# Optimization experiments

Hardware: AMD Instinct MI355X
Metric: run time of the kernel (lower is better)

Reference implementation:

```python
import jax, jax.numpy as jnp
import numpy as np

BN_EPS = 1e-5


def setup_inputs() -> dict:
    key = jax.random.key(0)
    ks = jax.random.split(key, 4)
    B, C, N = 16, 512, 4096
    Cr = C // 4
    x = jax.random.normal(ks[0], (B, C, N), dtype=jnp.float32)
    W1 = jax.random.normal(ks[1], (Cr, C), dtype=jnp.float32) * (1.0 / np.sqrt(C))
    W2 = jax.random.normal(ks[2], (C, Cr), dtype=jnp.float32) * (1.0 / np.sqrt(Cr))
    gamma = jnp.ones((Cr,), dtype=jnp.float32)
    beta = jnp.zeros((Cr,), dtype=jnp.float32)
    running_mean = jnp.zeros((Cr,), dtype=jnp.float32)
    running_var = jnp.ones((Cr,), dtype=jnp.float32)
    return {"x": x, "W1": W1, "gamma": gamma, "beta": beta,
            "running_mean": running_mean, "running_var": running_var, "W2": W2}


def reference(x, W1, gamma, beta, running_mean, running_var, W2):
    # att[b,c] = sum_j (x x^T)[b,c,j] = sum_n x[b,c,n] * s[b,n], s = colsum over channels.
    # Algebraically identical to bmm(x, x^T).sum(-1), avoids the [B,C,C] intermediate.
    s = jnp.sum(x, axis=1)                       # [B, N]
    att = jnp.einsum('bcn,bn->bc', x, s)         # [B, C]
    # 1x1 Conv1d (no bias) on a length-1 sequence == dense matmul.
    h = jnp.einsum('oc,bc->bo', W1, att)         # [B, C/4]
    # BatchNorm1d (inference mode, running statistics)
    h = gamma * (h - running_mean) * jax.lax.rsqrt(running_var + BN_EPS) + beta
    h = jax.nn.relu(h)
    a = jax.nn.sigmoid(jnp.einsum('oc,bc->bo', W2, h))  # [B, C]
    return x * a[:, :, None]                     # [B, C, N]
```

## Files before the change

### kernel.cpp

```cpp
#include <hip/hip_runtime.h>
#include <math.h>

#define B_   16
#define C_   512
#define CR_  128
#define N_   4096
#define N4_  (N_ / 4)
#define TN   32
#define TN4  (TN / 4)
#define SUBT 2
#define NTB  (N_ / TN / SUBT)

static constexpr float BN_EPS_F = 1e-5f;

typedef float vfloat4 __attribute__((ext_vector_type(4)));

__global__ __launch_bounds__(256) void k1f_att(
        const float* __restrict__ x,
        float* __restrict__ att_part) {
    const int ntb = blockIdx.x;
    const int b   = blockIdx.y;
    const int t   = threadIdx.x;
    const int g   = t >> 3;
    const int i   = t & 7;

    __shared__ vfloat4 s_red[32][8];
    __shared__ vfloat4 s_tile4[8];

    const vfloat4* x4 = (const vfloat4*)x;
    float dacc[16];
#pragma unroll
    for (int st = 0; st < 16; ++st) dacc[st] = 0.f;

    for (int sub = 0; sub < SUBT; ++sub) {
        const int nt = ntb * SUBT + sub;
        const vfloat4* base = x4 + (size_t)b * C_ * N4_ + (size_t)nt * TN4;
        vfloat4 v[16];
        vfloat4 sacc = {0.f, 0.f, 0.f, 0.f};
#pragma unroll
        for (int st = 0; st < 16; ++st) {
            v[st] = base[(size_t)(st * 32 + g) * N4_ + i];
            sacc += v[st];
        }
        if (sub) __syncthreads();
        s_red[g][i] = sacc;
        __syncthreads();
        if (t < 8) {
            vfloat4 acc = {0.f, 0.f, 0.f, 0.f};
#pragma unroll
            for (int g2 = 0; g2 < 32; ++g2)
                acc += s_red[g2][t];
            s_tile4[t] = acc;
        }
        __syncthreads();
        const vfloat4 sv = s_tile4[i];
#pragma unroll
        for (int st = 0; st < 16; ++st)
            dacc[st] += v[st].x * sv.x + v[st].y * sv.y
                      + v[st].z * sv.z + v[st].w * sv.w;
    }

#pragma unroll
    for (int st = 0; st < 16; ++st) {
        float d = dacc[st];
        d += __shfl_xor(d, 1, 64);
        d += __shfl_xor(d, 2, 64);
        d += __shfl_xor(d, 4, 64);
        dacc[st] = d;
    }
    if (i == 0) {
        float* dst = att_part + ((size_t)ntb * B_ + b) * C_;
#pragma unroll
        for (int st = 0; st < 16; ++st)
            dst[st * 32 + g] = dacc[st];
    }
}

__global__ void k3f(const float* __restrict__ att_part,
                    const float* __restrict__ W1,
                    const float* __restrict__ gamma,
                    const float* __restrict__ beta,
                    const float* __restrict__ rmean,
                    const float* __restrict__ rvar,
                    const float* __restrict__ W2,
                    float* __restrict__ a) {
    __shared__ float att_s[C_];
    __shared__ float h_s[CR_];
    const int b = blockIdx.x;
    const int t = threadIdx.x;

    {
        float a0 = 0.f, a1 = 0.f;
#pragma unroll 8
        for (int nb = 0; nb < NTB; ++nb) {
            const float* p = att_part + ((size_t)nb * B_ + b) * C_;
            a0 += p[t];
            a1 += p[t + 256];
        }
        att_s[t]       = a0;
        att_s[t + 256] = a1;
    }
    __syncthreads();

    if (t < CR_) {
        const float* w = W1 + (size_t)t * C_;
        float a0 = 0.f, a1 = 0.f, a2 = 0.f, a3 = 0.f;
#pragma unroll 4
        for (int c = 0; c < C_; c += 4) {
            a0 += w[c + 0] * att_s[c + 0];
            a1 += w[c + 1] * att_s[c + 1];
            a2 += w[c + 2] * att_s[c + 2];
            a3 += w[c + 3] * att_s[c + 3];
        }
        float acc = (a0 + a1) + (a2 + a3);
        float vv = gamma[t] * (acc - rmean[t]) * rsqrtf(rvar[t] + BN_EPS_F) + beta[t];
        h_s[t] = fmaxf(vv, 0.f);
    }
    __syncthreads();
#pragma unroll
    for (int j0 = 0; j0 < C_; j0 += 256) {
        const int j = j0 + t;
        const float* w = W2 + (size_t)j * CR_;
        float a0 = 0.f, a1 = 0.f, a2 = 0.f, a3 = 0.f;
#pragma unroll 4
        for (int k = 0; k < CR_; k += 4) {
            a0 += w[k + 0] * h_s[k + 0];
            a1 += w[k + 1] * h_s[k + 1];
            a2 += w[k + 2] * h_s[k + 2];
            a3 += w[k + 3] * h_s[k + 3];
        }
        float acc = (a0 + a1) + (a2 + a3);
        a[(size_t)b * C_ + j] = 1.f / (1.f + expf(-acc));
    }
}

__global__ __launch_bounds__(256) void k4_scale(
        const float* __restrict__ x,
        const float* __restrict__ a,
        float* __restrict__ out) {
    const int row = blockIdx.x;
    const float av = a[row];
    const vfloat4* xr = (const vfloat4*)x + (size_t)row * N4_;
    vfloat4* orow     = (vfloat4*)out     + (size_t)row * N4_;
#pragma unroll
    for (int it = 0; it < N4_ / 256; ++it) {
        const int idx = it * 256 + threadIdx.x;
        vfloat4 ov = xr[idx] * av;
        __builtin_nontemporal_store(ov, &orow[idx]);
    }
}

extern "C" void kernel_launch(void* const* d_in, const int* in_sizes, int n_in,
                              void* d_out, int out_size, void* d_ws, size_t ws_size,
                              hipStream_t stream) {
    const float* x     = (const float*)d_in[0];
    const float* W1    = (const float*)d_in[1];
    const float* gamma = (const float*)d_in[2];
    const float* beta  = (const float*)d_in[3];
    const float* rmean = (const float*)d_in[4];
    const float* rvar  = (const float*)d_in[5];
    const float* W2    = (const float*)d_in[6];
    float* out = (float*)d_out;

    float* ws       = (float*)d_ws;
    float* att_part = ws;
    float* a        = att_part + (size_t)NTB * B_ * C_;

    k1f_att<<<dim3(NTB, B_), 256, 0, stream>>>(x, att_part);
    k3f<<<dim3(B_), 256, 0, stream>>>(att_part, W1, gamma, beta, rmean, rvar, W2, a);
    k4_scale<<<dim3(B_ * C_), 256, 0, stream>>>(x, a, out);
}
```

Measured before the change: 88.29 us.

## Split squeeze-excite MLP into parallel reduction and wave-per-output kernels

Replaces the single 16-block MLP kernel with three kernels: a grid-wide reduction of partial attention sums, a wave-per-output W1 matvec with BN and ReLU, and a wave-per-output W2 matvec with sigmoid. The old kernel ran on only 16 blocks and serially read 64 partial rows per block, leaving most CUs idle on a latency-bound stage. The new version spreads the work across many blocks and uses coalesced weight reads with shuffle reductions, at the cost of two extra kernel launches and intermediate global round-trips.

```diff
diff --git a/kernel.cpp b/kernel.cpp
--- a/kernel.cpp
+++ b/kernel.cpp
@@ -76,62 +76,61 @@
     }
 }
 
-__global__ void k3f(const float* __restrict__ att_part,
-                    const float* __restrict__ W1,
-                    const float* __restrict__ gamma,
-                    const float* __restrict__ beta,
-                    const float* __restrict__ rmean,
-                    const float* __restrict__ rvar,
-                    const float* __restrict__ W2,
-                    float* __restrict__ a) {
-    __shared__ float att_s[C_];
-    __shared__ float h_s[CR_];
-    const int b = blockIdx.x;
-    const int t = threadIdx.x;
+__global__ __launch_bounds__(256) void k2r(
+        const float* __restrict__ att_part,
+        float* __restrict__ att) {
+    const int g = blockIdx.x * 256 + threadIdx.x;
+    float acc = 0.f;
+#pragma unroll 8
+    for (int nb = 0; nb < NTB; ++nb)
+        acc += att_part[(size_t)nb * (B_ * C_) + g];
+    att[g] = acc;
+}
 
-    {
-        float a0 = 0.f, a1 = 0.f;
-#pragma unroll 8
-        for (int nb = 0; nb < NTB; ++nb) {
-            const float* p = att_part + ((size_t)nb * B_ + b) * C_;
-            a0 += p[t];
-            a1 += p[t + 256];
-        }
-        att_s[t]       = a0;
-        att_s[t + 256] = a1;
+__global__ __launch_bounds__(256) void k3a(
+        const float* __restrict__ W1,
+        const float* __restrict__ att,
+        const float* __restrict__ gamma,
+        const float* __restrict__ beta,
+        const float* __restrict__ rmean,
+        const float* __restrict__ rvar,
+        float* __restrict__ h) {
+    const int wave = threadIdx.x >> 6;
+    const int lane = threadIdx.x & 63;
+    const int idx  = blockIdx.x * 4 + wave;
+    const int b = idx >> 7;
+    const int o = idx & (CR_ - 1);
+    const float* w  = W1  + (size_t)o * C_;
+    const float* at = att + (size_t)b * C_;
+    float acc = 0.f;
+#pragma unroll
+    for (int k = 0; k < C_ / 64; ++k)
+        acc += w[k * 64 + lane] * at[k * 64 + lane];
+#pragma unroll
+    for (int off = 32; off >= 1; off >>= 1)
+        acc += __shfl_down(acc, off, 64);
+    if (lane == 0) {
+        float v = gamma[o] * (acc - rmean[o]) * rsqrtf(rvar[o] + BN_EPS_F) + beta[o];
+        h[idx] = fmaxf(v, 0.f);
     }
-    __syncthreads();
+}
 
-    if (t < CR_) {
-        const float* w = W1 + (size_t)t * C_;
-        float a0 = 0.f, a1 = 0.f, a2 = 0.f, a3 = 0.f;
-#pragma unroll 4
-        for (int c = 0; c < C_; c += 4) {
-            a0 += w[c + 0] * att_s[c + 0];
-            a1 += w[c + 1] * att_s[c + 1];
-            a2 += w[c + 2] * att_s[c + 2];
-            a3 += w[c + 3] * att_s[c + 3];
-        }
-        float acc = (a0 + a1) + (a2 + a3);
-        float vv = gamma[t] * (acc - rmean[t]) * rsqrtf(rvar[t] + BN_EPS_F) + beta[t];
-        h_s[t] = fmaxf(vv, 0.f);
-    }
-    __syncthreads();
+__global__ __launch_bounds__(256) void k3b(
+        const float* __restrict__ W2,
+        const float* __restrict__ h,
+        float* __restrict__ a) {
+    const int wave = threadIdx.x >> 6;
+    const int lane = threadIdx.x & 63;
+    const int idx  = blockIdx.x * 4 + wave;
+    const int b = idx >> 9;
+    const int j = idx & (C_ - 1);
+    const float* w  = W2 + (size_t)j * CR_;
+    const float* hp = h  + (size_t)b * CR_;
+    float acc = w[lane] * hp[lane] + w[64 + lane] * hp[64 + lane];
 #pragma unroll
-    for (int j0 = 0; j0 < C_; j0 += 256) {
-        const int j = j0 + t;
-        const float* w = W2 + (size_t)j * CR_;
-        float a0 = 0.f, a1 = 0.f, a2 = 0.f, a3 = 0.f;
-#pragma unroll 4
-        for (int k = 0; k < CR_; k += 4) {
-            a0 += w[k + 0] * h_s[k + 0];
-            a1 += w[k + 1] * h_s[k + 1];
-            a2 += w[k + 2] * h_s[k + 2];
-            a3 += w[k + 3] * h_s[k + 3];
-        }
-        float acc = (a0 + a1) + (a2 + a3);
-        a[(size_t)b * C_ + j] = 1.f / (1.f + expf(-acc));
-    }
+    for (int off = 32; off >= 1; off >>= 1)
+        acc += __shfl_down(acc, off, 64);
+    if (lane == 0) a[idx] = 1.f / (1.f + expf(-acc));
 }
 
 __global__ __launch_bounds__(256) void k4_scale(
@@ -164,9 +163,13 @@
 
     float* ws       = (float*)d_ws;
     float* att_part = ws;
-    float* a        = att_part + (size_t)NTB * B_ * C_;
+    float* att      = att_part + (size_t)NTB * B_ * C_;
+    float* h        = att + (size_t)B_ * C_;
+    float* a        = h + (size_t)B_ * CR_;
 
     k1f_att<<<dim3(NTB, B_), 256, 0, stream>>>(x, att_part);
-    k3f<<<dim3(B_), 256, 0, stream>>>(att_part, W1, gamma, beta, rmean, rvar, W2, a);
+    k2r<<<dim3(B_ * C_ / 256), 256, 0, stream>>>(att_part, att);
+    k3a<<<dim3(B_ * CR_ / 4), 256, 0, stream>>>(W1, att, gamma, beta, rmean, rvar, h);
+    k3b<<<dim3(B_ * C_ / 4), 256, 0, stream>>>(W2, h, a);
     k4_scale<<<dim3(B_ * C_), 256, 0, stream>>>(x, a, out);
 }
```

Result: faster. 75.62 us (-14.4%).
